# Kernel optimization log

Hardware: AMD Instinct MI355X
Metric: run time of the kernel (lower is better)

The kernel has to match this reference:

```python
import jax, jax.numpy as jnp
import numpy as np

B, N, M, C = 8, 4096, 4096, 256
KS = 5          # dwc kernel size
FOCUS = 3.0     # focusing factor
EPS = 1e-6


def setup_inputs() -> dict:
    key = jax.random.key(0)
    ks = jax.random.split(key, 12)
    inp = {
        'query': jax.random.normal(ks[0], (B, N, C), jnp.float32),
        'key':   jax.random.normal(ks[1], (B, M, C), jnp.float32),
        'value': jax.random.normal(ks[2], (B, M, C), jnp.float32),
        'Wq':    jax.random.normal(ks[3], (C, C), jnp.float32) * 0.02,
        'Wk':    jax.random.normal(ks[4], (C, C), jnp.float32) * 0.02,
        'Wv':    jax.random.normal(ks[5], (C, C), jnp.float32) * 0.02,
        'Wproj': jax.random.normal(ks[6], (C, C), jnp.float32) * 0.02,
        'bproj': jax.random.normal(ks[7], (C,), jnp.float32) * 0.02,
        'dwc_w': jax.random.normal(ks[8], (C, 1, KS, KS), jnp.float32) * 0.02,
        'dwc_b': jax.random.normal(ks[9], (C,), jnp.float32) * 0.02,
        'scale': jax.random.normal(ks[10], (1, 1, C), jnp.float32) * 0.02,
        'H': 64,
        'W': 64,
    }
    return inp


def _dwconv(x, w, b):
    # x: (B, C, H, W), depthwise conv, SAME padding
    pad = KS // 2
    y = jax.lax.conv_general_dilated(
        x, w, window_strides=(1, 1), padding=[(pad, pad), (pad, pad)],
        dimension_numbers=('NCHW', 'OIHW', 'NCHW'), feature_group_count=C)
    return y + b[None, :, None, None]


def reference(query, key, value, Wq, Wk, Wv, Wproj, bproj, dwc_w, dwc_b, scale, H, W):
    q = jnp.einsum('bnc,dc->bnd', query, Wq)
    k = jnp.einsum('bmc,dc->bmd', key, Wk)
    v = jnp.einsum('bmc,dc->bmd', value, Wv)

    sc = jax.nn.softplus(scale)  # (1,1,C)
    q = (jax.nn.relu(q) + EPS) / sc
    k = (jax.nn.relu(k) + EPS) / sc

    q_norm = jnp.linalg.norm(q, axis=-1, keepdims=True)
    k_norm = jnp.linalg.norm(k, axis=-1, keepdims=True)
    # faithful to source: power then divide/multiply by the pre-power norm
    q = q ** FOCUS / q_norm * q_norm
    k = k ** FOCUS / k_norm * k_norm

    k_sum = k.sum(axis=1)                                   # (B, C)
    z_num = jnp.einsum('bnc,bc->bn', q, k_sum)              # (B, N)
    z = 1.0 / (z_num + EPS)

    kv = jnp.einsum('bmc,bmd->bcd', k, v)                   # (B, C, C)
    x = jnp.einsum('bnc,bcd->bnd', q, kv) * z[:, :, None]   # (B, N, C)

    xmap = x.transpose(0, 2, 1).reshape(x.shape[0], C, H, W)
    xmap = _dwconv(xmap, dwc_w, dwc_b)
    x = xmap.reshape(x.shape[0], C, H * W).transpose(0, 2, 1)

    x = x + q
    x = jnp.einsum('bnc,dc->bnd', x, Wproj) + bproj
    return x
```

## Files before the change

### kernel.cpp

```cpp
#include <hip/hip_runtime.h>
#include <math.h>
#include <stdint.h>

#define EPSF 1e-6f

typedef _Float16 half_t;
typedef _Float16 half8 __attribute__((ext_vector_type(8)));
typedef _Float16 half4 __attribute__((ext_vector_type(4)));
typedef float f32x4 __attribute__((ext_vector_type(4)));

#define MFMA16(A, B, C) __builtin_amdgcn_mfma_f32_16x16x32_f16(A, B, C, 0, 0, 0)

#define SBAR() __builtin_amdgcn_s_barrier()
#define WAIT_LGKM0()                                        \
  do {                                                      \
    asm volatile("s_waitcnt lgkmcnt(0)" ::: "memory");      \
    __builtin_amdgcn_sched_barrier(0);                      \
  } while (0)
#define WAIT_VM8_LGKM0()                                            \
  do {                                                              \
    asm volatile("s_waitcnt vmcnt(8) lgkmcnt(0)" ::: "memory");     \
    __builtin_amdgcn_sched_barrier(0);                              \
  } while (0)
#define WAIT_VM0_LGKM0()                                            \
  do {                                                              \
    asm volatile("s_waitcnt vmcnt(0) lgkmcnt(0)" ::: "memory");     \
    __builtin_amdgcn_sched_barrier(0);                              \
  } while (0)

__device__ __forceinline__ float softplusf(float x) {
  return (x > 20.f) ? x : log1pf(expf(x));
}

__device__ __forceinline__ void split4(const float4 v, half4& h, half4& l) {
  h.x = (half_t)v.x; l.x = (half_t)(v.x - (float)h.x);
  h.y = (half_t)v.y; l.y = (half_t)(v.y - (float)h.y);
  h.z = (half_t)v.z; l.z = (half_t)(v.z - (float)h.z);
  h.w = (half_t)v.w; l.w = (half_t)(v.w - (float)h.w);
}


__device__ __forceinline__ void stage_gld(const half_t* __restrict__ src, size_t rowbase,
                                          int ld, int k0, half_t* __restrict__ dst, int tid) {
#pragma unroll
  for (int r = 0; r < 2; ++r) {
    const int f = tid + r * 256;
    const half_t* g = src + (rowbase + (size_t)(f >> 2)) * (size_t)ld + k0 + (f & 3) * 8;
    const __attribute__((address_space(1))) unsigned int* gp =
        (const __attribute__((address_space(1))) unsigned int*)(uintptr_t)g;
    __attribute__((address_space(3))) unsigned int* lp =
        (__attribute__((address_space(3))) unsigned int*)(uintptr_t)(dst + f * 8);
    __builtin_amdgcn_global_load_lds(gp, lp, 16, 0, 0);
  }
}

__device__ __forceinline__ void frag_compute(const half_t* __restrict__ As_h,
                                             const half_t* __restrict__ As_l,
                                             const half_t* __restrict__ Bs_h,
                                             const half_t* __restrict__ Bs_l,
                                             f32x4 (&acc)[4][4], int lane, int wm, int wn) {
  const int lr = lane & 15, lg = lane >> 4;
  half8 ah[4], al[4], bh[4], bl[4];
#pragma unroll
  for (int i = 0; i < 4; ++i) {
    const int ar = (wm * 64 + i * 16 + lr) * 32 + lg * 8;
    ah[i] = *(const half8*)&As_h[ar];
    al[i] = *(const half8*)&As_l[ar];
    const int br = (wn * 64 + i * 16 + lr) * 32 + lg * 8;
    bh[i] = *(const half8*)&Bs_h[br];
    bl[i] = *(const half8*)&Bs_l[br];
  }
#pragma unroll
  for (int i = 0; i < 4; ++i)
#pragma unroll
    for (int j = 0; j < 4; ++j) {
      acc[i][j] = MFMA16(ah[i], bh[j], acc[i][j]);
      acc[i][j] = MFMA16(ah[i], bl[j], acc[i][j]);
      acc[i][j] = MFMA16(al[i], bh[j], acc[i][j]);
    }
}

__global__ void init_k(const float* __restrict__ scale, float* __restrict__ scs,
                       float* __restrict__ ksm) {
  const int i = blockIdx.x * 256 + threadIdx.x;
  if (i < 2048) ksm[i] = 0.f;
  if (i < 256) scs[i] = 1.f / softplusf(scale[i]);
}

__global__ __launch_bounds__(256) void proj_mfma(
    const float* __restrict__ query, const float* __restrict__ key,
    const float* __restrict__ value,
    const float* __restrict__ Wq, const float* __restrict__ Wk, const float* __restrict__ Wv,
    const float* __restrict__ rsc,
    half_t* __restrict__ qh, half_t* __restrict__ ql,
    half_t* __restrict__ khT, half_t* __restrict__ klT,
    half_t* __restrict__ vhT, half_t* __restrict__ vlT,
    float* __restrict__ ksm) {
  const int which = blockIdx.z;
  const int tid = threadIdx.x;
  const int lane = tid & 63, wave = tid >> 6, wm = wave >> 1, wn = wave & 1;
  const int lr = lane & 15, lg = lane >> 4;

  const float* srcA;
  const float* srcB;
  int rA0, rB0;
  if (which == 0) {
    srcA = Wq;    rA0 = blockIdx.y * 128;  srcB = query; rB0 = blockIdx.x * 128;
  } else if (which == 1) {
    srcA = key;   rA0 = blockIdx.x * 128;  srcB = Wk;    rB0 = blockIdx.y * 128;
  } else {
    srcA = value; rA0 = blockIdx.x * 128;  srcB = Wv;    rB0 = blockIdx.y * 128;
  }

  __shared__ __align__(16) half_t sm[32768];
  f32x4 acc[4][4] = {};
  float4 RA[2][4], RB[2][4];

  auto load_tile = [&](float4 (&ra)[4], float4 (&rb)[4], int ks) {
    const int k0 = ks * 32;
#pragma unroll
    for (int r = 0; r < 4; ++r) {
      const int f = tid + r * 256;
      const int row = f >> 3, c4 = f & 7;
      ra[r] = *(const float4*)&srcA[(size_t)(rA0 + row) * 256 + k0 + c4 * 4];
      rb[r] = *(const float4*)&srcB[(size_t)(rB0 + row) * 256 + k0 + c4 * 4];
    }
  };
  auto split_write = [&](const float4 (&ra)[4], const float4 (&rb)[4], half_t* base) {
#pragma unroll
    for (int r = 0; r < 4; ++r) {
      const int f = tid + r * 256;
      const int row = f >> 3, c4 = f & 7;
      half4 h, l;
      split4(ra[r], h, l);
      *(half4*)&base[row * 32 + c4 * 4] = h;
      *(half4*)&base[4096 + row * 32 + c4 * 4] = l;
      split4(rb[r], h, l);
      *(half4*)&base[8192 + row * 32 + c4 * 4] = h;
      *(half4*)&base[12288 + row * 32 + c4 * 4] = l;
    }
  };

  load_tile(RA[0], RB[0], 0);
  split_write(RA[0], RB[0], sm);
  load_tile(RA[1], RB[1], 1);
  WAIT_LGKM0();
  SBAR();
#pragma unroll
  for (int t = 0; t < 8; ++t) {
    if (t + 2 < 8) load_tile(RA[t & 1], RB[t & 1], t + 2);
    half_t* base = sm + (t & 1) * 16384;
    frag_compute(base, base + 4096, base + 8192, base + 12288, acc, lane, wm, wn);
    if (t + 1 < 8) split_write(RA[(t + 1) & 1], RB[(t + 1) & 1], sm + ((t + 1) & 1) * 16384);
    WAIT_LGKM0();
    SBAR();
  }

  if (which == 0) {
    const int dbase = rA0 + wm * 64;
    float rs[4][4];
#pragma unroll
    for (int i = 0; i < 4; ++i)
#pragma unroll
      for (int r = 0; r < 4; ++r) rs[i][r] = rsc[dbase + i * 16 + lg * 4 + r];
#pragma unroll
    for (int j = 0; j < 4; ++j) {
      const size_t nflat = (size_t)rB0 + wn * 64 + j * 16 + lr;
#pragma unroll
      for (int i = 0; i < 4; ++i) {
        half4 hv, lv;
#pragma unroll
        for (int r = 0; r < 4; ++r) {
          float v = acc[i][j][r];
          v = (fmaxf(v, 0.f) + EPSF) * rs[i][r];
          v = v * v * v;
          const half_t h = (half_t)v;
          hv[r] = h;
          lv[r] = (half_t)(v - (float)h);
        }
        const size_t o = nflat * 256 + dbase + i * 16 + lg * 4;
        *(half4*)&qh[o] = hv;
        *(half4*)&ql[o] = lv;
      }
    }
  } else {
    const int b = rA0 >> 12, m0 = rA0 & 4095;
    half_t* Thg = (which == 1) ? khT : vhT;
    half_t* Tlg = (which == 1) ? klT : vlT;
    const bool act = (which == 1);
    half_t* Tt = sm;
    half_t* Tl2 = sm + 4352;
    float kj[4] = {0.f, 0.f, 0.f, 0.f};
#pragma unroll
    for (int g = 0; g < 4; ++g) {
      if (wn == (g >> 1)) {
#pragma unroll
        for (int jj = 0; jj < 2; ++jj) {
          const int j = (g & 1) * 2 + jj;
          const int c = rB0 + wn * 64 + j * 16 + lr;
          const float rv = act ? rsc[c] : 1.f;
          const int crel = jj * 16 + lr;
#pragma unroll
          for (int i = 0; i < 4; ++i) {
            const int ml = wm * 64 + i * 16 + lg * 4;
            half4 hv, lv;
#pragma unroll
            for (int r = 0; r < 4; ++r) {
              float v = acc[i][j][r];
              if (act) { v = (fmaxf(v, 0.f) + EPSF) * rv; v = v * v * v; kj[j] += v; }
              const half_t h = (half_t)v;
              hv[r] = h;
              lv[r] = (half_t)(v - (float)h);
            }
            *(half4*)&Tt[crel * 136 + ml] = hv;
            *(half4*)&Tl2[crel * 136 + ml] = lv;
          }
        }
      }
      __syncthreads();
      {
        const int cr = tid >> 3, mm = (tid & 7) * 16;
        const size_t ga = ((size_t)(b * 256 + rB0 + g * 32 + cr)) * 4096 + m0 + mm;
        *(half8*)&Thg[ga]     = *(const half8*)&Tt[cr * 136 + mm];
        *(half8*)&Thg[ga + 8] = *(const half8*)&Tt[cr * 136 + mm + 8];
        *(half8*)&Tlg[ga]     = *(const half8*)&Tl2[cr * 136 + mm];
        *(half8*)&Tlg[ga + 8] = *(const half8*)&Tl2[cr * 136 + mm + 8];
      }
      __syncthreads();
    }
    if (act) {
#pragma unroll
      for (int j = 0; j < 4; ++j) {
        float s = kj[j];
        s += __shfl_xor(s, 16, 64);
        s += __shfl_xor(s, 32, 64);
        if (lg == 0) atomicAdd(&ksm[b * 256 + rB0 + wn * 64 + j * 16 + lr], s);
      }
    }
  }
}

__global__ __launch_bounds__(256) void kv_mfma(
    const half_t* __restrict__ vhT, const half_t* __restrict__ vlT,
    const half_t* __restrict__ khT, const half_t* __restrict__ klT,
    float* __restrict__ kvp) {
  const int b = blockIdx.z >> 3, s = blockIdx.z & 7;
  const int d0 = blockIdx.x * 128, c0 = blockIdx.y * 128;
  const int tid = threadIdx.x;
  __shared__ __align__(16) half_t sm[49152];
  f32x4 acc[4][4] = {};
  const int lane = tid & 63, wave = tid >> 6, wm = wave >> 1, wn = wave & 1;
  const int lr = lane & 15, lg = lane >> 4;
  const size_t arow = (size_t)b * 256 + d0, brow = (size_t)b * 256 + c0;

  auto stage = [&](int bi, int ks) {
    half_t* base = sm + bi * 16384;
    const int k0 = s * 512 + ks * 32;
    stage_gld(vhT, arow, 4096, k0, base, tid);
    stage_gld(vlT, arow, 4096, k0, base + 4096, tid);
    stage_gld(khT, brow, 4096, k0, base + 8192, tid);
    stage_gld(klT, brow, 4096, k0, base + 12288, tid);
  };

  stage(0, 0);
  stage(1, 1);
  WAIT_VM8_LGKM0();
  SBAR();
#pragma unroll
  for (int t = 0; t < 16; ++t) {
    if (t + 2 < 16) stage((t + 2) % 3, t + 2);
    half_t* base = sm + (t % 3) * 16384;
    frag_compute(base, base + 4096, base + 8192, base + 12288, acc, lane, wm, wn);
    if (t + 2 < 16) { WAIT_VM8_LGKM0(); } else { WAIT_VM0_LGKM0(); }
    SBAR();
  }

  float* outp = kvp + ((size_t)(b * 8 + s)) * 65536;
#pragma unroll
  for (int j = 0; j < 4; ++j) {
    const int c = c0 + wn * 64 + j * 16 + lr;
#pragma unroll
    for (int i = 0; i < 4; ++i) {
      const int d = d0 + wm * 64 + i * 16 + lg * 4;
#pragma unroll
      for (int r = 0; r < 4; ++r) outp[(size_t)(d + r) * 256 + c] = acc[i][j][r];
    }
  }
}

__global__ __launch_bounds__(256) void kv_red(const float* __restrict__ kvp,
                                              half_t* __restrict__ kvTh,
                                              half_t* __restrict__ kvTl) {
  const size_t idx = (size_t)blockIdx.x * 256 + threadIdx.x;
  const int b = (int)(idx >> 16);
  const int dc = (int)(idx & 65535);
  float s = 0.f;
#pragma unroll
  for (int t = 0; t < 8; ++t) s += kvp[((size_t)(b * 8 + t)) * 65536 + dc];
  const half_t h = (half_t)s;
  kvTh[idx] = h;
  kvTl[idx] = (half_t)(s - (float)h);
}

__global__ __launch_bounds__(256) void x1_mfma(
    const half_t* __restrict__ qh, const half_t* __restrict__ ql,
    const half_t* __restrict__ kvTh, const half_t* __restrict__ kvTl,
    const float* __restrict__ ksm, float* __restrict__ xt) {
  const int b = blockIdx.z, n0 = blockIdx.x * 128, d0t = blockIdx.y * 128;
  const int tid = threadIdx.x;
  __shared__ __align__(16) half_t sm[49152];
  __shared__ float zden[128];
  f32x4 acc[4][4] = {};
  const int lane = tid & 63, wave = tid >> 6, wm = wave >> 1, wn = wave & 1;
  const int lr = lane & 15, lg = lane >> 4;
  const size_t arow = (size_t)b * 4096 + n0, brow = (size_t)b * 256 + d0t;

  auto stage = [&](int bi, int ks) {
    half_t* base = sm + bi * 16384;
    const int k0 = ks * 32;
    stage_gld(qh, arow, 256, k0, base, tid);
    stage_gld(ql, arow, 256, k0, base + 4096, tid);
    stage_gld(kvTh, brow, 256, k0, base + 8192, tid);
    stage_gld(kvTl, brow, 256, k0, base + 12288, tid);
  };

  stage(0, 0);
  stage(1, 1);
  WAIT_VM8_LGKM0();
  SBAR();
  float zpart = 0.f;
  const int zrow = tid >> 1, zkh = tid & 1;
#pragma unroll
  for (int t = 0; t < 8; ++t) {
    if (t + 2 < 8) stage((t + 2) % 3, t + 2);
    half_t* base = sm + (t % 3) * 16384;
    frag_compute(base, base + 4096, base + 8192, base + 12288, acc, lane, wm, wn);
    {
      const half_t* hp = base + zrow * 32 + zkh * 16;
      const half_t* lp = base + 4096 + zrow * 32 + zkh * 16;
      const half8 h0 = *(const half8*)&hp[0];
      const half8 h1 = *(const half8*)&hp[8];
      const half8 l0 = *(const half8*)&lp[0];
      const half8 l1 = *(const half8*)&lp[8];
      const float* ksp = ksm + b * 256 + t * 32 + zkh * 16;
#pragma unroll
      for (int u = 0; u < 8; ++u) {
        zpart += ((float)h0[u] + (float)l0[u]) * ksp[u];
        zpart += ((float)h1[u] + (float)l1[u]) * ksp[8 + u];
      }
    }
    if (t + 2 < 8) { WAIT_VM8_LGKM0(); } else { WAIT_VM0_LGKM0(); }
    SBAR();
  }

  zpart += __shfl_xor(zpart, 1, 64);
  if ((tid & 1) == 0) zden[zrow] = zpart;
  __syncthreads();

#pragma unroll
  for (int i = 0; i < 4; ++i) {
    const int nl = wm * 64 + i * 16 + lg * 4;
    float zr[4];
#pragma unroll
    for (int r = 0; r < 4; ++r) zr[r] = 1.f / (zden[nl + r] + EPSF);
#pragma unroll
    for (int j = 0; j < 4; ++j) {
      const int d = d0t + wn * 64 + j * 16 + lr;
      *(float4*)&xt[((size_t)b * 256 + d) * 4096 + n0 + nl] =
          make_float4(acc[i][j][0] * zr[0], acc[i][j][1] * zr[1],
                      acc[i][j][2] * zr[2], acc[i][j][3] * zr[3]);
    }
  }
}

__global__ __launch_bounds__(256) void dwconv_kernel(const float* __restrict__ xt,
                                                     const float* __restrict__ w,
                                                     const float* __restrict__ bias,
                                                     float* __restrict__ xc) {
  const int bc = blockIdx.x;
  const int c = bc & 255;
  const float* plane = xt + (size_t)bc * 4096;
  float* oplane = xc + (size_t)bc * 4096;

  __shared__ float Ls[68][72];
  const int tid = threadIdx.x;
  for (int i = tid; i < 68 * 72; i += 256) ((float*)Ls)[i] = 0.f;
  __syncthreads();
#pragma unroll
  for (int p = 0; p < 4; ++p) {
    const int f = tid + p * 256;
    const int y = f >> 4, x4 = f & 15;
    *(float4*)&Ls[2 + y][4 + x4 * 4] = *(const float4*)&plane[y * 64 + x4 * 4];
  }
  __syncthreads();

  float wreg[25];
#pragma unroll
  for (int t = 0; t < 25; ++t) wreg[t] = w[c * 25 + t];
  const float bv = bias[c];

  const int x = tid & 63, ys0 = (tid >> 6) * 16;
  float win[5][5];
#pragma unroll
  for (int r = 0; r < 5; ++r)
#pragma unroll
    for (int cx = 0; cx < 5; ++cx) win[r][cx] = Ls[ys0 + r][x + 2 + cx];

  for (int yy = 0; yy < 16; ++yy) {
    float s = bv;
#pragma unroll
    for (int ky = 0; ky < 5; ++ky)
#pragma unroll
      for (int kx = 0; kx < 5; ++kx) s = fmaf(win[ky][kx], wreg[ky * 5 + kx], s);
    oplane[(ys0 + yy) * 64 + x] = s;
    if (yy < 15) {
#pragma unroll
      for (int r = 0; r < 4; ++r)
#pragma unroll
        for (int cx = 0; cx < 5; ++cx) win[r][cx] = win[r + 1][cx];
#pragma unroll
      for (int cx = 0; cx < 5; ++cx) win[4][cx] = Ls[ys0 + yy + 5][x + 2 + cx];
    }
  }
}

__global__ __launch_bounds__(256) void final_mfma(
    const half_t* __restrict__ qh, const half_t* __restrict__ ql,
    const float* __restrict__ xc, const float* __restrict__ Wp,
    const float* __restrict__ bp, float* __restrict__ outp) {
  const int b = blockIdx.z, n0 = blockIdx.x * 128, dd0 = blockIdx.y * 128;
  const int tid = threadIdx.x;
  __shared__ __align__(16) half_t As_h[4096], As_l[4096], Bs_h[4096], Bs_l[4096];
  __shared__ __align__(16) float Xs[32 * 130];
  f32x4 acc[4][4] = {};
  const int lane = tid & 63, wave = tid >> 6, wm = wave >> 1, wn = wave & 1;
  const int lr = lane & 15, lg = lane >> 4;

  float4 rxs[4], rwp[4];
  half8 rqh[2][2], rql[2][2];

  auto load_xw = [&](int ks) {
    const int k0 = ks * 32;
#pragma unroll
    for (int r = 0; r < 4; ++r) {
      const int f = tid + r * 256;
      rxs[r] = *(const float4*)&xc[((size_t)b * 256 + k0 + (f >> 5)) * 4096 + n0 + (f & 31) * 4];
      rwp[r] = *(const float4*)&Wp[(size_t)(dd0 + (f >> 3)) * 256 + k0 + (f & 7) * 4];
    }
  };

  load_xw(0);
#pragma unroll
  for (int r = 0; r < 2; ++r) {
    const int f = tid + r * 256;
    const size_t qoff = ((size_t)b * 4096 + n0 + (f >> 2)) * 256 + (f & 3) * 8;
    rqh[0][r] = *(const half8*)&qh[qoff];
    rql[0][r] = *(const half8*)&ql[qoff];
  }

#pragma unroll
  for (int t = 0; t < 8; ++t) {
#pragma unroll
    for (int r = 0; r < 4; ++r) {
      const int f = tid + r * 256;
      const int cc = f >> 5, n4 = f & 31;
      *(float2*)&Xs[cc * 130 + n4 * 4] = make_float2(rxs[r].x, rxs[r].y);
      *(float2*)&Xs[cc * 130 + n4 * 4 + 2] = make_float2(rxs[r].z, rxs[r].w);
      half4 h, l;
      split4(rwp[r], h, l);
      *(half4*)&Bs_h[(f >> 3) * 32 + (f & 7) * 4] = h;
      *(half4*)&Bs_l[(f >> 3) * 32 + (f & 7) * 4] = l;
    }
    WAIT_LGKM0();
    SBAR();
#pragma unroll
    for (int r = 0; r < 2; ++r) {
      const int f = tid + r * 256, row = f >> 2, ch = f & 3;
      const half8 h8 = rqh[t & 1][r];
      const half8 l8 = rql[t & 1][r];
      half8 oh, ol;
#pragma unroll
      for (int u = 0; u < 8; ++u) {
        const float v = (float)h8[u] + (float)l8[u] + Xs[(ch * 8 + u) * 130 + row];
        const half_t h = (half_t)v;
        oh[u] = h;
        ol[u] = (half_t)(v - (float)h);
      }
      *(half8*)&As_h[row * 32 + ch * 8] = oh;
      *(half8*)&As_l[row * 32 + ch * 8] = ol;
    }
    WAIT_LGKM0();
    SBAR();
    if (t + 1 < 8) {
      load_xw(t + 1);
      const int k0n = (t + 1) * 32;
#pragma unroll
      for (int r = 0; r < 2; ++r) {
        const int f = tid + r * 256;
        const size_t qoff = ((size_t)b * 4096 + n0 + (f >> 2)) * 256 + k0n + (f & 3) * 8;
        rqh[(t + 1) & 1][r] = *(const half8*)&qh[qoff];
        rql[(t + 1) & 1][r] = *(const half8*)&ql[qoff];
      }
    }
    frag_compute(As_h, As_l, Bs_h, Bs_l, acc, lane, wm, wn);
    WAIT_LGKM0();
    SBAR();
  }

#pragma unroll
  for (int j = 0; j < 4; ++j) {
    const int dd = dd0 + wn * 64 + j * 16 + lr;
    const float bb = bp[dd];
#pragma unroll
    for (int i = 0; i < 4; ++i) {
      const size_t rowg = (size_t)b * 4096 + n0 + wm * 64 + i * 16 + lg * 4;
#pragma unroll
      for (int r = 0; r < 4; ++r) outp[(rowg + r) * 256 + dd] = acc[i][j][r] + bb;
    }
  }
}

extern "C" void kernel_launch(void* const* d_in, const int* in_sizes, int n_in,
                              void* d_out, int out_size, void* d_ws, size_t ws_size,
                              hipStream_t stream) {
  const float* query = (const float*)d_in[0];
  const float* key   = (const float*)d_in[1];
  const float* value = (const float*)d_in[2];
  const float* Wq    = (const float*)d_in[3];
  const float* Wk    = (const float*)d_in[4];
  const float* Wv    = (const float*)d_in[5];
  const float* Wproj = (const float*)d_in[6];
  const float* bproj = (const float*)d_in[7];
  const float* dwc_w = (const float*)d_in[8];
  const float* dwc_b = (const float*)d_in[9];
  const float* scale = (const float*)d_in[10];

  const size_t U = (size_t)8 * 4096 * 256;
  half_t* qh  = (half_t*)d_ws;
  half_t* ql  = qh + U;
  half_t* khT = ql + U;
  half_t* klT = khT + U;
  half_t* vhT = klT + U;
  half_t* vlT = vhT + U;
  float*  kvp = (float*)(vlT + U);
  half_t* kvTh = (half_t*)(kvp + (size_t)8 * 8 * 65536);
  half_t* kvTl = kvTh + (size_t)8 * 65536;
  float*  ksm = (float*)(kvTl + (size_t)8 * 65536);
  float*  zbuf = ksm + 8 * 256;
  float*  scs  = zbuf + 32768;
  float* xt = (float*)khT;
  float* xc = (float*)vhT;
  float* outp = (float*)d_out;

  const dim3 blk(256);
  init_k<<<dim3(8), blk, 0, stream>>>(scale, scs, ksm);
  proj_mfma<<<dim3(256, 2, 3), blk, 0, stream>>>(query, key, value, Wq, Wk, Wv, scs,
                                                 qh, ql, khT, klT, vhT, vlT, ksm);
  kv_mfma<<<dim3(2, 2, 64), blk, 0, stream>>>(vhT, vlT, khT, klT, kvp);
  kv_red<<<dim3(2048), blk, 0, stream>>>(kvp, kvTh, kvTl);
  x1_mfma<<<dim3(32, 2, 8), blk, 0, stream>>>(qh, ql, kvTh, kvTl, ksm, xt);
  dwconv_kernel<<<dim3(2048), blk, 0, stream>>>(xt, dwc_w, dwc_b, xc);
  final_mfma<<<dim3(32, 2, 8), blk, 0, stream>>>(qh, ql, xc, Wproj, bproj, outp);
}
```

Measured before the change: 300.4 us.

## Replace multi-stage LDS pipelines with single buffer to raise occupancy

```diff
diff --git a/kernel.cpp b/kernel.cpp
--- a/kernel.cpp
+++ b/kernel.cpp
@@ -16,11 +16,6 @@
   do {                                                      \
     asm volatile("s_waitcnt lgkmcnt(0)" ::: "memory");      \
     __builtin_amdgcn_sched_barrier(0);                      \
-  } while (0)
-#define WAIT_VM8_LGKM0()                                            \
-  do {                                                              \
-    asm volatile("s_waitcnt vmcnt(8) lgkmcnt(0)" ::: "memory");     \
-    __builtin_amdgcn_sched_barrier(0);                              \
   } while (0)
 #define WAIT_VM0_LGKM0()                                            \
   do {                                                              \
@@ -87,7 +82,7 @@
   if (i < 256) scs[i] = 1.f / softplusf(scale[i]);
 }
 
-__global__ __launch_bounds__(256) void proj_mfma(
+__global__ __launch_bounds__(256, 4) void proj_mfma(
     const float* __restrict__ query, const float* __restrict__ key,
     const float* __restrict__ value,
     const float* __restrict__ Wq, const float* __restrict__ Wk, const float* __restrict__ Wv,
@@ -112,47 +107,48 @@
     srcA = value; rA0 = blockIdx.x * 128;  srcB = Wv;    rB0 = blockIdx.y * 128;
   }
 
-  __shared__ __align__(16) half_t sm[32768];
+  __shared__ __align__(16) half_t sm[16384];
   f32x4 acc[4][4] = {};
-  float4 RA[2][4], RB[2][4];
-
-  auto load_tile = [&](float4 (&ra)[4], float4 (&rb)[4], int ks) {
+  float4 RA[4], RB[4];
+
+  auto load_tile = [&](int ks) {
     const int k0 = ks * 32;
 #pragma unroll
     for (int r = 0; r < 4; ++r) {
       const int f = tid + r * 256;
       const int row = f >> 3, c4 = f & 7;
-      ra[r] = *(const float4*)&srcA[(size_t)(rA0 + row) * 256 + k0 + c4 * 4];
-      rb[r] = *(const float4*)&srcB[(size_t)(rB0 + row) * 256 + k0 + c4 * 4];
+      RA[r] = *(const float4*)&srcA[(size_t)(rA0 + row) * 256 + k0 + c4 * 4];
+      RB[r] = *(const float4*)&srcB[(size_t)(rB0 + row) * 256 + k0 + c4 * 4];
     }
   };
-  auto split_write = [&](const float4 (&ra)[4], const float4 (&rb)[4], half_t* base) {
+  auto split_write = [&]() {
 #pragma unroll
     for (int r = 0; r < 4; ++r) {
       const int f = tid + r * 256;
       const int row = f >> 3, c4 = f & 7;
       half4 h, l;
-      split4(ra[r], h, l);
-      *(half4*)&base[row * 32 + c4 * 4] = h;
-      *(half4*)&base[4096 + row * 32 + c4 * 4] = l;
-      split4(rb[r], h, l);
-      *(half4*)&base[8192 + row * 32 + c4 * 4] = h;
-      *(half4*)&base[12288 + row * 32 + c4 * 4] = l;
+      split4(RA[r], h, l);
+      *(half4*)&sm[row * 32 + c4 * 4] = h;
+      *(half4*)&sm[4096 + row * 32 + c4 * 4] = l;
+      split4(RB[r], h, l);
+      *(half4*)&sm[8192 + row * 32 + c4 * 4] = h;
+      *(half4*)&sm[12288 + row * 32 + c4 * 4] = l;
     }
   };
 
-  load_tile(RA[0], RB[0], 0);
-  split_write(RA[0], RB[0], sm);
-  load_tile(RA[1], RB[1], 1);
+  load_tile(0);
+  split_write();
   WAIT_LGKM0();
   SBAR();
 #pragma unroll
   for (int t = 0; t < 8; ++t) {
-    if (t + 2 < 8) load_tile(RA[t & 1], RB[t & 1], t + 2);
-    half_t* base = sm + (t & 1) * 16384;
-    frag_compute(base, base + 4096, base + 8192, base + 12288, acc, lane, wm, wn);
-    if (t + 1 < 8) split_write(RA[(t + 1) & 1], RB[(t + 1) & 1], sm + ((t + 1) & 1) * 16384);
-    WAIT_LGKM0();
+    if (t + 1 < 8) load_tile(t + 1);
+    frag_compute(sm, sm + 4096, sm + 8192, sm + 12288, acc, lane, wm, wn);
+    SBAR();
+    if (t + 1 < 8) {
+      split_write();
+      WAIT_LGKM0();
+    }
     SBAR();
   }
 
@@ -247,31 +243,22 @@
   const int b = blockIdx.z >> 3, s = blockIdx.z & 7;
   const int d0 = blockIdx.x * 128, c0 = blockIdx.y * 128;
   const int tid = threadIdx.x;
-  __shared__ __align__(16) half_t sm[49152];
+  __shared__ __align__(16) half_t sm[16384];
   f32x4 acc[4][4] = {};
   const int lane = tid & 63, wave = tid >> 6, wm = wave >> 1, wn = wave & 1;
   const int lr = lane & 15, lg = lane >> 4;
   const size_t arow = (size_t)b * 256 + d0, brow = (size_t)b * 256 + c0;
 
-  auto stage = [&](int bi, int ks) {
-    half_t* base = sm + bi * 16384;
-    const int k0 = s * 512 + ks * 32;
-    stage_gld(vhT, arow, 4096, k0, base, tid);
-    stage_gld(vlT, arow, 4096, k0, base + 4096, tid);
-    stage_gld(khT, brow, 4096, k0, base + 8192, tid);
-    stage_gld(klT, brow, 4096, k0, base + 12288, tid);
-  };
-
-  stage(0, 0);
-  stage(1, 1);
-  WAIT_VM8_LGKM0();
-  SBAR();
 #pragma unroll
   for (int t = 0; t < 16; ++t) {
-    if (t + 2 < 16) stage((t + 2) % 3, t + 2);
-    half_t* base = sm + (t % 3) * 16384;
-    frag_compute(base, base + 4096, base + 8192, base + 12288, acc, lane, wm, wn);
-    if (t + 2 < 16) { WAIT_VM8_LGKM0(); } else { WAIT_VM0_LGKM0(); }
+    const int k0 = s * 512 + t * 32;
+    stage_gld(vhT, arow, 4096, k0, sm, tid);
+    stage_gld(vlT, arow, 4096, k0, sm + 4096, tid);
+    stage_gld(khT, brow, 4096, k0, sm + 8192, tid);
+    stage_gld(klT, brow, 4096, k0, sm + 12288, tid);
+    WAIT_VM0_LGKM0();
+    SBAR();
+    frag_compute(sm, sm + 4096, sm + 8192, sm + 12288, acc, lane, wm, wn);
     SBAR();
   }
 
@@ -308,36 +295,28 @@
     const float* __restrict__ ksm, float* __restrict__ xt) {
   const int b = blockIdx.z, n0 = blockIdx.x * 128, d0t = blockIdx.y * 128;
   const int tid = threadIdx.x;
-  __shared__ __align__(16) half_t sm[49152];
+  __shared__ __align__(16) half_t sm[16384];
   __shared__ float zden[128];
   f32x4 acc[4][4] = {};
   const int lane = tid & 63, wave = tid >> 6, wm = wave >> 1, wn = wave & 1;
   const int lr = lane & 15, lg = lane >> 4;
   const size_t arow = (size_t)b * 4096 + n0, brow = (size_t)b * 256 + d0t;
 
-  auto stage = [&](int bi, int ks) {
-    half_t* base = sm + bi * 16384;
-    const int k0 = ks * 32;
-    stage_gld(qh, arow, 256, k0, base, tid);
-    stage_gld(ql, arow, 256, k0, base + 4096, tid);
-    stage_gld(kvTh, brow, 256, k0, base + 8192, tid);
-    stage_gld(kvTl, brow, 256, k0, base + 12288, tid);
-  };
-
-  stage(0, 0);
-  stage(1, 1);
-  WAIT_VM8_LGKM0();
-  SBAR();
   float zpart = 0.f;
   const int zrow = tid >> 1, zkh = tid & 1;
 #pragma unroll
   for (int t = 0; t < 8; ++t) {
-    if (t + 2 < 8) stage((t + 2) % 3, t + 2);
-    half_t* base = sm + (t % 3) * 16384;
-    frag_compute(base, base + 4096, base + 8192, base + 12288, acc, lane, wm, wn);
+    const int k0 = t * 32;
+    stage_gld(qh, arow, 256, k0, sm, tid);
+    stage_gld(ql, arow, 256, k0, sm + 4096, tid);
+    stage_gld(kvTh, brow, 256, k0, sm + 8192, tid);
+    stage_gld(kvTl, brow, 256, k0, sm + 12288, tid);
+    WAIT_VM0_LGKM0();
+    SBAR();
+    frag_compute(sm, sm + 4096, sm + 8192, sm + 12288, acc, lane, wm, wn);
     {
-      const half_t* hp = base + zrow * 32 + zkh * 16;
-      const half_t* lp = base + 4096 + zrow * 32 + zkh * 16;
+      const half_t* hp = sm + zrow * 32 + zkh * 16;
+      const half_t* lp = sm + 4096 + zrow * 32 + zkh * 16;
       const half8 h0 = *(const half8*)&hp[0];
       const half8 h1 = *(const half8*)&hp[8];
       const half8 l0 = *(const half8*)&lp[0];
@@ -349,7 +328,6 @@
         zpart += ((float)h1[u] + (float)l1[u]) * ksp[8 + u];
       }
     }
-    if (t + 2 < 8) { WAIT_VM8_LGKM0(); } else { WAIT_VM0_LGKM0(); }
     SBAR();
   }
 
```

Result: slower. 460.4 us (+53.3%).
